# Performance work log

Hardware: AMD Instinct MI355X
Metric: run time of the kernel (lower is better)

## Reference

```python
import jax, jax.numpy as jnp
import numpy as np

N_NODES = 1000000
N_EDGES = 32000000
NUM_GRAPHS = 1024


def setup_inputs() -> dict:
    key = jax.random.key(0)
    k1, k2, k3, k4, k5 = jax.random.split(key, 5)
    x = jax.random.normal(k1, (N_NODES, 1), dtype=jnp.float32)
    W = jax.random.normal(k2, (1, 1), dtype=jnp.float32)
    b = jax.random.normal(k3, (1,), dtype=jnp.float32)
    edge_index = jax.random.randint(k4, (2, N_EDGES), 0, N_NODES, dtype=jnp.int64)
    batch = jnp.sort(jax.random.randint(k5, (N_NODES,), 0, NUM_GRAPHS, dtype=jnp.int64))
    return {"x": x, "W": W, "b": b, "edge_index": edge_index, "batch": batch}


def reference(x, W, b, edge_index, batch):
    src, dst = edge_index[0], edge_index[1]
    # SimpleConv (default sum aggregation): out[i] = sum_{(j->i) in E} x[j]
    agg = jax.ops.segment_sum(x[src], dst, num_segments=N_NODES)  # [N,1]
    h = jax.nn.relu(agg)
    # global_mean_pool over graph ids
    sums = jax.ops.segment_sum(h, batch, num_segments=NUM_GRAPHS)  # [G,1]
    counts = jax.ops.segment_sum(jnp.ones((N_NODES,), dtype=h.dtype), batch,
                                 num_segments=NUM_GRAPHS)  # [G]
    pooled = sums / jnp.maximum(counts, 1.0)[:, None]
    # Linear(1 -> 1): y = pooled @ W^T + b
    return pooled @ W.T + b
```

## Files before the change

kernel.cpp:

```cpp
#include <hip/hip_runtime.h>

#define N_NODES    1000000
#define N_EDGES    32000000
#define NUM_GRAPHS 1024

typedef int          vint4  __attribute__((ext_vector_type(4)));
typedef unsigned int uint32;
typedef unsigned int vuint4 __attribute__((ext_vector_type(4)));

#define BUCKET_SHIFT 12
#define BUCKET_NODES (1 << BUCKET_SHIFT)
#define NBUCKETS     245

#define T1_NCHUNK   512
#define T1_BLOCK    512
#define T1_EDGES_PER_CHUNK (N_EDGES / T1_NCHUNK)
#define T1_QUADS    (T1_EDGES_PER_CHUNK / 4)
#define T1_ROUNDS   ((T1_QUADS + T1_BLOCK - 1) / T1_BLOCK)
#define SCAP        64
#define SLAB_CAP    368

#define T2_CAP      136192
#define T2_NCHUNK   512
#define T2_EPC      (N_EDGES / T2_NCHUNK)

__global__ __launch_bounds__(T1_BLOCK)
void slab_scatter(const int* __restrict__ src,
                  const int* __restrict__ dst,
                  uint32* __restrict__ slab,
                  uint32* __restrict__ fcnt_g,
                  uint32* __restrict__ ecnt_g) {
    __shared__ uint32 stage[NBUCKETS][SCAP];
    __shared__ uint32 rpos[NBUCKETS];
    __shared__ uint32 ecnt[NBUCKETS];
    __shared__ uint32 flushed[NBUCKETS];
    __shared__ uint32 carry[NBUCKETS];

    const int tid = threadIdx.x;
    const int w   = blockIdx.x;
    const vint4* d4 = (const vint4*)(dst + (size_t)w * T1_EDGES_PER_CHUNK);
    const vint4* s4 = (const vint4*)(src + (size_t)w * T1_EDGES_PER_CHUNK);

    for (int b = tid; b < NBUCKETS; b += T1_BLOCK) {
        rpos[b] = 0; ecnt[b] = 0; flushed[b] = 0; carry[b] = 0;
    }
    __syncthreads();

    const int grp    = tid >> 4;
    const int lane16 = tid & 15;

    for (int r = 0; r < T1_ROUNDS; ++r) {
        int q = r * T1_BLOCK + tid;
        if (q < T1_QUADS) {
            vint4 d = d4[q];
            vint4 s = s4[q];
            #pragma unroll
            for (int k = 0; k < 4; ++k) {
                uint32 dd = (uint32)(k == 0 ? d.x : k == 1 ? d.y : k == 2 ? d.z : d.w);
                uint32 ss = (uint32)(k == 0 ? s.x : k == 1 ? s.y : k == 2 ? s.z : s.w);
                uint32 b  = dd >> BUCKET_SHIFT;
                uint32 v  = ((dd & (BUCKET_NODES - 1)) << 20) | ss;
                uint32 c  = carry[b] + atomicAdd(&rpos[b], 1u);
                if (c < SCAP) {
                    stage[b][c] = v;
                } else {
                    uint32 e = atomicAdd(&ecnt[b], 1u);
                    slab[((size_t)b * T1_NCHUNK + w) * SLAB_CAP + (SLAB_CAP - 1 - e)] = v;
                }
            }
        }
        __syncthreads();
        for (int b = grp; b < NBUCKETS; b += 32) {
            uint32 tot = carry[b] + rpos[b];
            if (tot > SCAP) tot = SCAP;
            uint32 lines = tot >> 4;
            uint32 rem   = tot & 15u;
            uint32 fl    = flushed[b];
            uint32* dp = slab + ((size_t)b * T1_NCHUNK + w) * SLAB_CAP + fl;
            for (uint32 l = 0; l < lines; ++l)
                dp[l * 16 + lane16] = stage[b][l * 16 + lane16];
            if (lines) {
                uint32 mv = 0;
                if (lane16 < rem) mv = stage[b][lines * 16 + lane16];
                if (lane16 < rem) stage[b][lane16] = mv;
            }
            if (lane16 == 0) {
                flushed[b] = fl + lines * 16;
                carry[b]   = rem;
                rpos[b]    = 0;
            }
        }
        __syncthreads();
    }
    for (int b = grp; b < NBUCKETS; b += 32) {
        uint32 rem = carry[b];
        uint32 fl  = flushed[b];
        uint32* dp = slab + ((size_t)b * T1_NCHUNK + w) * SLAB_CAP + fl;
        if (lane16 < rem) dp[lane16] = stage[b][lane16];
        if (lane16 == 0) {
            fcnt_g[(size_t)b * T1_NCHUNK + w] = fl + rem;
            ecnt_g[(size_t)b * T1_NCHUNK + w] = ecnt[b];
        }
    }
}

__global__ __launch_bounds__(1024)
void slab_reduce(const uint32* __restrict__ slab,
                 const uint32* __restrict__ fcnt_g,
                 const uint32* __restrict__ ecnt_g,
                 const float* __restrict__ x,
                 const int* __restrict__ batch,
                 float* __restrict__ sums,
                 float* __restrict__ counts) {
    __shared__ float acc[BUCKET_NODES];
    const int b = blockIdx.x;
    const int tid = threadIdx.x;
    for (int n = tid; n < BUCKET_NODES; n += 1024) acc[n] = 0.0f;
    __syncthreads();

    const int wv = tid >> 6, lane = tid & 63;
    for (int w = wv; w < T1_NCHUNK; w += 16) {
        size_t cell = (size_t)b * T1_NCHUNK + w;
        uint32 fc = fcnt_g[cell];
        uint32 ec = ecnt_g[cell];
        const uint32* base = slab + cell * SLAB_CAP;
        const vuint4* b4 = (const vuint4*)base;
        uint32 nq = fc >> 2;
        for (uint32 i = lane; i < nq; i += 64) {
            vuint4 v = b4[i];
            atomicAdd(&acc[v.x >> 20], x[v.x & 0xFFFFFu]);
            atomicAdd(&acc[v.y >> 20], x[v.y & 0xFFFFFu]);
            atomicAdd(&acc[v.z >> 20], x[v.z & 0xFFFFFu]);
            atomicAdd(&acc[v.w >> 20], x[v.w & 0xFFFFFu]);
        }
        for (uint32 i = nq * 4 + lane; i < fc; i += 64) {
            uint32 v = base[i];
            atomicAdd(&acc[v >> 20], x[v & 0xFFFFFu]);
        }
        for (uint32 i = lane; i < ec; i += 64) {
            uint32 v = base[SLAB_CAP - 1 - i];
            atomicAdd(&acc[v >> 20], x[v & 0xFFFFFu]);
        }
    }
    __syncthreads();

    const int node0 = b << BUCKET_SHIFT;
    for (int n = tid; n < BUCKET_NODES; n += 1024) {
        int i = node0 + n;
        float h = 0.0f;
        int g = -1;
        if (i < N_NODES) {
            h = fmaxf(acc[n], 0.0f);
            g = batch[i];
        }
        int g0 = __shfl(g, 0);
        if (__all(g == g0)) {
            #pragma unroll
            for (int off = 32; off > 0; off >>= 1)
                h += __shfl_down(h, off);
            if ((tid & 63) == 0 && g0 >= 0) {
                atomicAdd(&sums[g0], h);
                atomicAdd(&counts[g0], 64.0f);
            }
        } else if (g >= 0) {
            atomicAdd(&sums[g], h);
            atomicAdd(&counts[g], 1.0f);
        }
    }
}

__global__ void finalize_kernel(const float* __restrict__ sums,
                                const float* __restrict__ counts,
                                const float* __restrict__ W,
                                const float* __restrict__ b,
                                float* __restrict__ out) {
    int g = blockIdx.x * blockDim.x + threadIdx.x;
    if (g < NUM_GRAPHS) {
        float pooled = sums[g] / fmaxf(counts[g], 1.0f);
        out[g] = pooled * W[0] + b[0];
    }
}

__global__ __launch_bounds__(1024)
void bucket_scatter(const int* __restrict__ src,
                    const int* __restrict__ dst,
                    uint32* __restrict__ sorted,
                    uint32* __restrict__ gpos) {
    __shared__ uint32 hist[NBUCKETS];
    __shared__ uint32 pos[NBUCKETS];
    const int tid = threadIdx.x;
    const size_t base = (size_t)blockIdx.x * T2_EPC;
    for (int b = tid; b < NBUCKETS; b += 1024) hist[b] = 0;
    __syncthreads();
    const vint4* d4 = (const vint4*)(dst + base);
    const vint4* s4 = (const vint4*)(src + base);
    const int nvec = T2_EPC / 4;
    for (int i = tid; i < nvec; i += 1024) {
        vint4 d = d4[i];
        atomicAdd(&hist[(uint32)d.x >> BUCKET_SHIFT], 1u);
        atomicAdd(&hist[(uint32)d.y >> BUCKET_SHIFT], 1u);
        atomicAdd(&hist[(uint32)d.z >> BUCKET_SHIFT], 1u);
        atomicAdd(&hist[(uint32)d.w >> BUCKET_SHIFT], 1u);
    }
    __syncthreads();
    for (int b = tid; b < NBUCKETS; b += 1024)
        pos[b] = atomicAdd(&gpos[b], hist[b]);
    __syncthreads();
    for (int i = tid; i < nvec; i += 1024) {
        vint4 d = d4[i];
        vint4 s = s4[i];
        #pragma unroll
        for (int k = 0; k < 4; ++k) {
            uint32 dd = (uint32)(k == 0 ? d.x : k == 1 ? d.y : k == 2 ? d.z : d.w);
            uint32 ss = (uint32)(k == 0 ? s.x : k == 1 ? s.y : k == 2 ? s.z : s.w);
            uint32 b = dd >> BUCKET_SHIFT, dl = dd & (BUCKET_NODES - 1);
            uint32 slot = atomicAdd(&pos[b], 1u);
            if (slot < T2_CAP) sorted[(size_t)b * T2_CAP + slot] = (dl << 20) | ss;
        }
    }
}

__global__ __launch_bounds__(1024)
void bucket_reduce(const uint32* __restrict__ sorted,
                   const uint32* __restrict__ gpos,
                   const float* __restrict__ x,
                   const int* __restrict__ batch,
                   float* __restrict__ sums,
                   float* __restrict__ counts) {
    __shared__ float acc[BUCKET_NODES];
    const int b = blockIdx.x;
    const int tid = threadIdx.x;
    for (int n = tid; n < BUCKET_NODES; n += 1024) acc[n] = 0.0f;
    __syncthreads();
    uint32 cnt = gpos[b];
    if (cnt > T2_CAP) cnt = T2_CAP;
    const uint32* reg = sorted + (size_t)b * T2_CAP;
    const vuint4* r4 = (const vuint4*)reg;
    const uint32 nvec = cnt / 4;
    for (uint32 i = tid; i < nvec; i += 1024) {
        vuint4 v = r4[i];
        atomicAdd(&acc[v.x >> 20], x[v.x & 0xFFFFFu]);
        atomicAdd(&acc[v.y >> 20], x[v.y & 0xFFFFFu]);
        atomicAdd(&acc[v.z >> 20], x[v.z & 0xFFFFFu]);
        atomicAdd(&acc[v.w >> 20], x[v.w & 0xFFFFFu]);
    }
    for (uint32 i = nvec * 4 + tid; i < cnt; i += 1024) {
        uint32 v = reg[i];
        atomicAdd(&acc[v >> 20], x[v & 0xFFFFFu]);
    }
    __syncthreads();
    const int node0 = b << BUCKET_SHIFT;
    for (int n = tid; n < BUCKET_NODES; n += 1024) {
        int i = node0 + n;
        float h = 0.0f;
        int g = -1;
        if (i < N_NODES) {
            h = fmaxf(acc[n], 0.0f);
            g = batch[i];
        }
        int g0 = __shfl(g, 0);
        if (__all(g == g0)) {
            #pragma unroll
            for (int off = 32; off > 0; off >>= 1)
                h += __shfl_down(h, off);
            if ((tid & 63) == 0 && g0 >= 0) {
                atomicAdd(&sums[g0], h);
                atomicAdd(&counts[g0], 64.0f);
            }
        } else if (g >= 0) {
            atomicAdd(&sums[g], h);
            atomicAdd(&counts[g], 1.0f);
        }
    }
}

__global__ void scatter_edges_dev(const vint4* __restrict__ src4,
                                  const vint4* __restrict__ dst4,
                                  const float* __restrict__ x,
                                  float* __restrict__ agg) {
    int t = blockIdx.x * blockDim.x + threadIdx.x;
    if (t < N_EDGES / 4) {
        vint4 s = __builtin_nontemporal_load(&src4[t]);
        vint4 d = __builtin_nontemporal_load(&dst4[t]);
        atomicAdd(&agg[d.x], x[s.x]);
        atomicAdd(&agg[d.y], x[s.y]);
        atomicAdd(&agg[d.z], x[s.z]);
        atomicAdd(&agg[d.w], x[s.w]);
    }
}

__global__ void pool_nodes_kernel(const float* __restrict__ agg,
                                  const int* __restrict__ batch,
                                  float* __restrict__ sums,
                                  float* __restrict__ counts) {
    int i = blockIdx.x * blockDim.x + threadIdx.x;
    float h = 0.0f;
    int g = -1;
    if (i < N_NODES) {
        h = fmaxf(agg[i], 0.0f);
        g = batch[i];
    }
    int g0 = __shfl(g, 0);
    if (__all(g == g0)) {
        #pragma unroll
        for (int off = 32; off > 0; off >>= 1)
            h += __shfl_down(h, off);
        if ((threadIdx.x & 63) == 0 && g0 >= 0) {
            atomicAdd(&sums[g0], h);
            atomicAdd(&counts[g0], 64.0f);
        }
    } else if (g >= 0) {
        atomicAdd(&sums[g], h);
        atomicAdd(&counts[g], 1.0f);
    }
}

extern "C" void kernel_launch(void* const* d_in, const int* in_sizes, int n_in,
                              void* d_out, int out_size, void* d_ws, size_t ws_size,
                              hipStream_t stream) {
    const float* x     = (const float*)d_in[0];
    const float* W     = (const float*)d_in[1];
    const float* b     = (const float*)d_in[2];
    const int*   edge  = (const int*)d_in[3];
    const int*   batch = (const int*)d_in[4];
    float* out = (float*)d_out;

    const int* src = edge;
    const int* dst = edge + N_EDGES;

    const size_t ncells     = (size_t)NBUCKETS * T1_NCHUNK;
    const size_t slab_elems = ncells * SLAB_CAP;
    const size_t need1 = (slab_elems + 2 * ncells + 2 * NUM_GRAPHS) * 4;
    const size_t t2_elems = (size_t)NBUCKETS * T2_CAP;
    const size_t need2 = (t2_elems + 256 + 2 * NUM_GRAPHS) * 4;

    if (ws_size >= need1) {
        uint32* slab   = (uint32*)d_ws;
        uint32* fcnt_g = slab + slab_elems;
        uint32* ecnt_g = fcnt_g + ncells;
        float*  sums   = (float*)(ecnt_g + ncells);
        float*  counts = sums + NUM_GRAPHS;
        (void)hipMemsetAsync(sums, 0, 2 * NUM_GRAPHS * 4, stream);

        slab_scatter<<<T1_NCHUNK, T1_BLOCK, 0, stream>>>(src, dst, slab, fcnt_g, ecnt_g);
        slab_reduce<<<NBUCKETS, 1024, 0, stream>>>(slab, fcnt_g, ecnt_g, x, batch, sums, counts);
        finalize_kernel<<<(NUM_GRAPHS + 255) / 256, 256, 0, stream>>>(sums, counts, W, b, out);
    } else if (ws_size >= need2) {
        uint32* sorted = (uint32*)d_ws;
        uint32* gpos   = sorted + t2_elems;
        float*  sums   = (float*)(gpos + 256);
        float*  counts = sums + NUM_GRAPHS;
        (void)hipMemsetAsync(gpos, 0, (256 + 2 * NUM_GRAPHS) * 4, stream);

        bucket_scatter<<<T2_NCHUNK, 1024, 0, stream>>>(src, dst, sorted, gpos);
        bucket_reduce<<<NBUCKETS, 1024, 0, stream>>>(sorted, gpos, x, batch, sums, counts);
        finalize_kernel<<<(NUM_GRAPHS + 255) / 256, 256, 0, stream>>>(sums, counts, W, b, out);
    } else {
        float* agg    = (float*)d_ws;
        float* sums   = agg + N_NODES;
        float* counts = sums + NUM_GRAPHS;
        (void)hipMemsetAsync(d_ws, 0, ((size_t)N_NODES + 2 * NUM_GRAPHS) * 4, stream);

        int nthreads = N_EDGES / 4;
        scatter_edges_dev<<<(nthreads + 255) / 256, 256, 0, stream>>>(
            (const vint4*)src, (const vint4*)dst, x, agg);
        pool_nodes_kernel<<<(N_NODES + 255) / 256, 256, 0, stream>>>(agg, batch, sums, counts);
        finalize_kernel<<<(NUM_GRAPHS + 255) / 256, 256, 0, stream>>>(sums, counts, W, b, out);
    }
}
```

Before: 622.5 us.

## Split per-bucket slab reduction across four workgroups with global atomic merge

Adds a new reduce path that splits each node bucket's 512 slab cells across four workgroups, so there are 4x as many blocks (980 instead of 245) to fill the GPU. Each block accumulates partial sums in LDS and merges them into a global agg array with atomics. A separate pool_nodes_kernel then does the relu and mean-pool. This costs an extra memset, an extra kernel launch, global atomics and a second pass over the aggregated nodes. The path only runs if the workspace is large enough for the added agg buffer.

```diff
diff --git a/kernel.cpp b/kernel.cpp
--- a/kernel.cpp
+++ b/kernel.cpp
@@ -19,6 +19,9 @@
 #define T1_ROUNDS   ((T1_QUADS + T1_BLOCK - 1) / T1_BLOCK)
 #define SCAP        64
 #define SLAB_CAP    368
+
+#define RSPLIT        4
+#define CELLS_PER_WG  (T1_NCHUNK / RSPLIT)
 
 #define T2_CAP      136192
 #define T2_NCHUNK   512
@@ -105,6 +108,62 @@
 }
 
 __global__ __launch_bounds__(1024)
+void slab_reduce2(const uint32* __restrict__ slab,
+                  const uint32* __restrict__ fcnt_g,
+                  const uint32* __restrict__ ecnt_g,
+                  const float* __restrict__ x,
+                  float* __restrict__ agg) {
+    __shared__ float  acc[BUCKET_NODES];
+    __shared__ uint32 fc_s[CELLS_PER_WG];
+    __shared__ uint32 ec_s[CELLS_PER_WG];
+
+    const int b    = blockIdx.x / RSPLIT;
+    const int part = blockIdx.x % RSPLIT;
+    const int tid  = threadIdx.x;
+
+    for (int n = tid; n < BUCKET_NODES; n += 1024) acc[n] = 0.0f;
+    if (tid < CELLS_PER_WG) {
+        size_t cell = (size_t)b * T1_NCHUNK + (size_t)part * CELLS_PER_WG + tid;
+        fc_s[tid] = fcnt_g[cell];
+        ec_s[tid] = ecnt_g[cell];
+    }
+    __syncthreads();
+
+    const int wv = tid >> 6, lane = tid & 63;
+    for (int c = wv; c < CELLS_PER_WG; c += 16) {
+        const int w = part * CELLS_PER_WG + c;
+        const size_t cell = (size_t)b * T1_NCHUNK + w;
+        const uint32 fc = fc_s[c];
+        const uint32 ec = ec_s[c];
+        const uint32* base = slab + cell * SLAB_CAP;
+        const vuint4* b4 = (const vuint4*)base;
+        const uint32 nq = fc >> 2;
+        for (uint32 i = lane; i < nq; i += 64) {
+            vuint4 v = __builtin_nontemporal_load(&b4[i]);
+            atomicAdd(&acc[v.x >> 20], x[v.x & 0xFFFFFu]);
+            atomicAdd(&acc[v.y >> 20], x[v.y & 0xFFFFFu]);
+            atomicAdd(&acc[v.z >> 20], x[v.z & 0xFFFFFu]);
+            atomicAdd(&acc[v.w >> 20], x[v.w & 0xFFFFFu]);
+        }
+        for (uint32 i = nq * 4 + lane; i < fc; i += 64) {
+            uint32 v = __builtin_nontemporal_load(&base[i]);
+            atomicAdd(&acc[v >> 20], x[v & 0xFFFFFu]);
+        }
+        for (uint32 i = lane; i < ec; i += 64) {
+            uint32 v = base[SLAB_CAP - 1 - i];
+            atomicAdd(&acc[v >> 20], x[v & 0xFFFFFu]);
+        }
+    }
+    __syncthreads();
+
+    const int node0 = b << BUCKET_SHIFT;
+    for (int n = tid; n < BUCKET_NODES; n += 1024) {
+        float v = acc[n];
+        if (v != 0.0f) atomicAdd(&agg[node0 + n], v);
+    }
+}
+
+__global__ __launch_bounds__(1024)
 void slab_reduce(const uint32* __restrict__ slab,
                  const uint32* __restrict__ fcnt_g,
                  const uint32* __restrict__ ecnt_g,
@@ -330,11 +389,26 @@
 
     const size_t ncells     = (size_t)NBUCKETS * T1_NCHUNK;
     const size_t slab_elems = ncells * SLAB_CAP;
+    const size_t nagg       = (size_t)NBUCKETS * BUCKET_NODES;
+    const size_t need0 = (slab_elems + 2 * ncells + nagg + 2 * NUM_GRAPHS) * 4;
     const size_t need1 = (slab_elems + 2 * ncells + 2 * NUM_GRAPHS) * 4;
     const size_t t2_elems = (size_t)NBUCKETS * T2_CAP;
     const size_t need2 = (t2_elems + 256 + 2 * NUM_GRAPHS) * 4;
 
-    if (ws_size >= need1) {
+    if (ws_size >= need0) {
+        uint32* slab   = (uint32*)d_ws;
+        uint32* fcnt_g = slab + slab_elems;
+        uint32* ecnt_g = fcnt_g + ncells;
+        float*  agg    = (float*)(ecnt_g + ncells);
+        float*  sums   = agg + nagg;
+        float*  counts = sums + NUM_GRAPHS;
+        (void)hipMemsetAsync(agg, 0, (nagg + 2 * NUM_GRAPHS) * 4, stream);
+
+        slab_scatter<<<T1_NCHUNK, T1_BLOCK, 0, stream>>>(src, dst, slab, fcnt_g, ecnt_g);
+        slab_reduce2<<<NBUCKETS * RSPLIT, 1024, 0, stream>>>(slab, fcnt_g, ecnt_g, x, agg);
+        pool_nodes_kernel<<<(N_NODES + 255) / 256, 256, 0, stream>>>(agg, batch, sums, counts);
+        finalize_kernel<<<(NUM_GRAPHS + 255) / 256, 256, 0, stream>>>(sums, counts, W, b, out);
+    } else if (ws_size >= need1) {
         uint32* slab   = (uint32*)d_ws;
         uint32* fcnt_g = slab + slab_elems;
         uint32* ecnt_g = fcnt_g + ncells;
```

Result: slower. 650.1 us (+4.4%).

## Split slab reduction across four workgroups per bucket and add nontemporal memory ops

Applied to the files above, without the earlier changes.

The slab reduce now launches four workgroups per bucket, each handling a quarter of the chunk cells and interleaving four cells per wave. Each workgroup atomically adds its shared-memory partials into a global per-node aggregate, and a separate pooling kernel then applies relu and the per-graph mean. The goal is more parallelism and memory-level overlap in the reduce, which previously ran with only 245 workgroups. The scatter kernel now processes two quads per thread per round, uses nontemporal loads and stores, and adds overflow guards. The cost is an extra memset, global float atomics, an extra kernel launch and a larger workspace requirement.

```diff
diff --git a/kernel.cpp b/kernel.cpp
--- a/kernel.cpp
+++ b/kernel.cpp
@@ -16,9 +16,13 @@
 #define T1_BLOCK    512
 #define T1_EDGES_PER_CHUNK (N_EDGES / T1_NCHUNK)
 #define T1_QUADS    (T1_EDGES_PER_CHUNK / 4)
-#define T1_ROUNDS   ((T1_QUADS + T1_BLOCK - 1) / T1_BLOCK)
+#define T1_QPR      (2 * T1_BLOCK)
+#define T1_ROUNDS   ((T1_QUADS + T1_QPR - 1) / T1_QPR)
 #define SCAP        64
 #define SLAB_CAP    368
+
+#define RSPLIT        4
+#define CELLS_PER_WG  (T1_NCHUNK / RSPLIT)
 
 #define T2_CAP      136192
 #define T2_NCHUNK   512
@@ -50,25 +54,41 @@
     const int lane16 = tid & 15;
 
     for (int r = 0; r < T1_ROUNDS; ++r) {
-        int q = r * T1_BLOCK + tid;
-        if (q < T1_QUADS) {
-            vint4 d = d4[q];
-            vint4 s = s4[q];
-            #pragma unroll
-            for (int k = 0; k < 4; ++k) {
-                uint32 dd = (uint32)(k == 0 ? d.x : k == 1 ? d.y : k == 2 ? d.z : d.w);
-                uint32 ss = (uint32)(k == 0 ? s.x : k == 1 ? s.y : k == 2 ? s.z : s.w);
-                uint32 b  = dd >> BUCKET_SHIFT;
-                uint32 v  = ((dd & (BUCKET_NODES - 1)) << 20) | ss;
-                uint32 c  = carry[b] + atomicAdd(&rpos[b], 1u);
-                if (c < SCAP) {
-                    stage[b][c] = v;
-                } else {
-                    uint32 e = atomicAdd(&ecnt[b], 1u);
-                    slab[((size_t)b * T1_NCHUNK + w) * SLAB_CAP + (SLAB_CAP - 1 - e)] = v;
-                }
-            }
-        }
+        const int q0 = r * T1_QPR + tid;
+        const int q1 = q0 + T1_BLOCK;
+        const bool ok0 = q0 < T1_QUADS;
+        const bool ok1 = q1 < T1_QUADS;
+        vint4 d0, s0, d1, s1;
+        if (ok0) { d0 = __builtin_nontemporal_load(&d4[q0]);
+                   s0 = __builtin_nontemporal_load(&s4[q0]); }
+        if (ok1) { d1 = __builtin_nontemporal_load(&d4[q1]);
+                   s1 = __builtin_nontemporal_load(&s4[q1]); }
+
+#define SCAT4(dd4, ss4)                                                        \
+        {                                                                      \
+            _Pragma("unroll")                                                  \
+            for (int k = 0; k < 4; ++k) {                                      \
+                uint32 dd = (uint32)(k == 0 ? dd4.x : k == 1 ? dd4.y :         \
+                                     k == 2 ? dd4.z : dd4.w);                  \
+                uint32 ss = (uint32)(k == 0 ? ss4.x : k == 1 ? ss4.y :         \
+                                     k == 2 ? ss4.z : ss4.w);                  \
+                uint32 b  = dd >> BUCKET_SHIFT;                                \
+                uint32 v  = ((dd & (BUCKET_NODES - 1)) << 20) | ss;            \
+                uint32 c  = carry[b] + atomicAdd(&rpos[b], 1u);                \
+                if (c < SCAP) {                                                \
+                    stage[b][c] = v;                                           \
+                } else {                                                       \
+                    uint32 e = atomicAdd(&ecnt[b], 1u);                        \
+                    if (e < SLAB_CAP)          \
+                        __builtin_nontemporal_store(v,                         \
+                            &slab[((size_t)b * T1_NCHUNK + w) * SLAB_CAP       \
+                                  + (SLAB_CAP - 1 - e)]);                      \
+                }                                                              \
+            }                                                                  \
+        }
+        if (ok0) SCAT4(d0, s0)
+        if (ok1) SCAT4(d1, s1)
+#undef SCAT4
         __syncthreads();
         for (int b = grp; b < NBUCKETS; b += 32) {
             uint32 tot = carry[b] + rpos[b];
@@ -76,9 +96,12 @@
             uint32 lines = tot >> 4;
             uint32 rem   = tot & 15u;
             uint32 fl    = flushed[b];
+            uint32 maxl  = (SLAB_CAP > fl) ? ((SLAB_CAP - fl) >> 4) : 0u;
+            if (lines > maxl) lines = maxl;
             uint32* dp = slab + ((size_t)b * T1_NCHUNK + w) * SLAB_CAP + fl;
             for (uint32 l = 0; l < lines; ++l)
-                dp[l * 16 + lane16] = stage[b][l * 16 + lane16];
+                __builtin_nontemporal_store(stage[b][l * 16 + lane16],
+                                            &dp[l * 16 + lane16]);
             if (lines) {
                 uint32 mv = 0;
                 if (lane16 < rem) mv = stage[b][lines * 16 + lane16];
@@ -96,54 +119,188 @@
         uint32 rem = carry[b];
         uint32 fl  = flushed[b];
         uint32* dp = slab + ((size_t)b * T1_NCHUNK + w) * SLAB_CAP + fl;
-        if (lane16 < rem) dp[lane16] = stage[b][lane16];
+        if (lane16 < rem && fl + lane16 < SLAB_CAP)
+            __builtin_nontemporal_store(stage[b][lane16], &dp[lane16]);
         if (lane16 == 0) {
-            fcnt_g[(size_t)b * T1_NCHUNK + w] = fl + rem;
+            uint32 fc = fl + rem;
+            fcnt_g[(size_t)b * T1_NCHUNK + w] = fc > SLAB_CAP ? SLAB_CAP : fc;
             ecnt_g[(size_t)b * T1_NCHUNK + w] = ecnt[b];
         }
     }
 }
 
 __global__ __launch_bounds__(1024)
-void slab_reduce(const uint32* __restrict__ slab,
-                 const uint32* __restrict__ fcnt_g,
-                 const uint32* __restrict__ ecnt_g,
-                 const float* __restrict__ x,
-                 const int* __restrict__ batch,
-                 float* __restrict__ sums,
-                 float* __restrict__ counts) {
+void slab_reduce2(const uint32* __restrict__ slab,
+                  const uint32* __restrict__ fcnt_g,
+                  const uint32* __restrict__ ecnt_g,
+                  const float* __restrict__ x,
+                  float* __restrict__ agg) {
+    __shared__ float  acc[BUCKET_NODES];
+    __shared__ uint32 fc_s[CELLS_PER_WG];
+    __shared__ uint32 ec_s[CELLS_PER_WG];
+
+    const int b    = blockIdx.x / RSPLIT;
+    const int part = blockIdx.x % RSPLIT;
+    const int tid  = threadIdx.x;
+
+    for (int n = tid; n < BUCKET_NODES; n += 1024) acc[n] = 0.0f;
+    if (tid < CELLS_PER_WG) {
+        size_t cell = (size_t)b * T1_NCHUNK + (size_t)part * CELLS_PER_WG + tid;
+        uint32 fc = fcnt_g[cell];
+        uint32 ec = ecnt_g[cell];
+        if (fc > SLAB_CAP) fc = SLAB_CAP;
+        if (ec > SLAB_CAP) ec = SLAB_CAP;
+        fc_s[tid] = fc;
+        ec_s[tid] = ec;
+    }
+    __syncthreads();
+
+    const int wv = tid >> 6, lane = tid & 63;
+    for (int cp = wv; cp < CELLS_PER_WG; cp += 64) {
+        const int cA = cp, cB = cp + 16, cC = cp + 32, cD = cp + 48;
+        const uint32 fcA = fc_s[cA], fcB = fc_s[cB], fcC = fc_s[cC], fcD = fc_s[cD];
+        const uint32* baseA = slab + ((size_t)b * T1_NCHUNK + part * CELLS_PER_WG + cA) * SLAB_CAP;
+        const uint32* baseB = slab + ((size_t)b * T1_NCHUNK + part * CELLS_PER_WG + cB) * SLAB_CAP;
+        const uint32* baseC = slab + ((size_t)b * T1_NCHUNK + part * CELLS_PER_WG + cC) * SLAB_CAP;
+        const uint32* baseD = slab + ((size_t)b * T1_NCHUNK + part * CELLS_PER_WG + cD) * SLAB_CAP;
+        const uint32 nqA = fcA >> 2, nqB = fcB >> 2, nqC = fcC >> 2, nqD = fcD >> 2;
+        uint32 nqM = nqA;
+        if (nqB > nqM) nqM = nqB;
+        if (nqC > nqM) nqM = nqC;
+        if (nqD > nqM) nqM = nqD;
+
+        for (uint32 i = lane; i < nqM; i += 64) {
+            const bool aOK = i < nqA, bOK = i < nqB, cOK = i < nqC, dOK = i < nqD;
+            vuint4 va, vb, vc, vd;
+            if (aOK) va = __builtin_nontemporal_load(&((const vuint4*)baseA)[i]);
+            if (bOK) vb = __builtin_nontemporal_load(&((const vuint4*)baseB)[i]);
+            if (cOK) vc = __builtin_nontemporal_load(&((const vuint4*)baseC)[i]);
+            if (dOK) vd = __builtin_nontemporal_load(&((const vuint4*)baseD)[i]);
+            float xa0, xa1, xa2, xa3, xb0, xb1, xb2, xb3;
+            float xc0, xc1, xc2, xc3, xd0, xd1, xd2, xd3;
+            if (aOK) { xa0 = x[va.x & 0xFFFFFu]; xa1 = x[va.y & 0xFFFFFu];
+                       xa2 = x[va.z & 0xFFFFFu]; xa3 = x[va.w & 0xFFFFFu]; }
+            if (bOK) { xb0 = x[vb.x & 0xFFFFFu]; xb1 = x[vb.y & 0xFFFFFu];
+                       xb2 = x[vb.z & 0xFFFFFu]; xb3 = x[vb.w & 0xFFFFFu]; }
+            if (cOK) { xc0 = x[vc.x & 0xFFFFFu]; xc1 = x[vc.y & 0xFFFFFu];
+                       xc2 = x[vc.z & 0xFFFFFu]; xc3 = x[vc.w & 0xFFFFFu]; }
+            if (dOK) { xd0 = x[vd.x & 0xFFFFFu]; xd1 = x[vd.y & 0xFFFFFu];
+                       xd2 = x[vd.z & 0xFFFFFu]; xd3 = x[vd.w & 0xFFFFFu]; }
+            if (aOK) { atomicAdd(&acc[va.x >> 20], xa0); atomicAdd(&acc[va.y >> 20], xa1);
+                       atomicAdd(&acc[va.z >> 20], xa2); atomicAdd(&acc[va.w >> 20], xa3); }
+            if (bOK) { atomicAdd(&acc[vb.x >> 20], xb0); atomicAdd(&acc[vb.y >> 20], xb1);
+                       atomicAdd(&acc[vb.z >> 20], xb2); atomicAdd(&acc[vb.w >> 20], xb3); }
+            if (cOK) { atomicAdd(&acc[vc.x >> 20], xc0); atomicAdd(&acc[vc.y >> 20], xc1);
+                       atomicAdd(&acc[vc.z >> 20], xc2); atomicAdd(&acc[vc.w >> 20], xc3); }
+            if (dOK) { atomicAdd(&acc[vd.x >> 20], xd0); atomicAdd(&acc[vd.y >> 20], xd1);
+                       atomicAdd(&acc[vd.z >> 20], xd2); atomicAdd(&acc[vd.w >> 20], xd3); }
+        }
+#define REM(base, fc, ec)                                                      \
+        {                                                                      \
+            for (uint32 i = ((fc) & ~3u) + lane; i < (fc); i += 64) {          \
+                uint32 v = __builtin_nontemporal_load(&(base)[i]);             \
+                atomicAdd(&acc[v >> 20], x[v & 0xFFFFFu]);                     \
+            }                                                                  \
+            for (uint32 i = lane; i < (ec); i += 64) {                         \
+                uint32 v = (base)[SLAB_CAP - 1 - i];                           \
+                atomicAdd(&acc[v >> 20], x[v & 0xFFFFFu]);                     \
+            }                                                                  \
+        }
+        REM(baseA, fcA, ec_s[cA])
+        REM(baseB, fcB, ec_s[cB])
+        REM(baseC, fcC, ec_s[cC])
+        REM(baseD, fcD, ec_s[cD])
+#undef REM
+    }
+    __syncthreads();
+
+    const int node0 = b << BUCKET_SHIFT;
+    for (int n = tid; n < BUCKET_NODES; n += 1024) {
+        float v = acc[n];
+        if (v != 0.0f) atomicAdd(&agg[node0 + n], v);
+    }
+}
+
+__global__ void finalize_kernel(const float* __restrict__ sums,
+                                const float* __restrict__ counts,
+                                const float* __restrict__ W,
+                                const float* __restrict__ b,
+                                float* __restrict__ out) {
+    int g = blockIdx.x * blockDim.x + threadIdx.x;
+    if (g < NUM_GRAPHS) {
+        float pooled = sums[g] / fmaxf(counts[g], 1.0f);
+        out[g] = pooled * W[0] + b[0];
+    }
+}
+
+__global__ __launch_bounds__(1024)
+void bucket_scatter(const int* __restrict__ src,
+                    const int* __restrict__ dst,
+                    uint32* __restrict__ sorted,
+                    uint32* __restrict__ gpos) {
+    __shared__ uint32 hist[NBUCKETS];
+    __shared__ uint32 pos[NBUCKETS];
+    const int tid = threadIdx.x;
+    const size_t base = (size_t)blockIdx.x * T2_EPC;
+    for (int b = tid; b < NBUCKETS; b += 1024) hist[b] = 0;
+    __syncthreads();
+    const vint4* d4 = (const vint4*)(dst + base);
+    const vint4* s4 = (const vint4*)(src + base);
+    const int nvec = T2_EPC / 4;
+    for (int i = tid; i < nvec; i += 1024) {
+        vint4 d = d4[i];
+        atomicAdd(&hist[(uint32)d.x >> BUCKET_SHIFT], 1u);
+        atomicAdd(&hist[(uint32)d.y >> BUCKET_SHIFT], 1u);
+        atomicAdd(&hist[(uint32)d.z >> BUCKET_SHIFT], 1u);
+        atomicAdd(&hist[(uint32)d.w >> BUCKET_SHIFT], 1u);
+    }
+    __syncthreads();
+    for (int b = tid; b < NBUCKETS; b += 1024)
+        pos[b] = atomicAdd(&gpos[b], hist[b]);
+    __syncthreads();
+    for (int i = tid; i < nvec; i += 1024) {
+        vint4 d = d4[i];
+        vint4 s = s4[i];
+        #pragma unroll
+        for (int k = 0; k < 4; ++k) {
+            uint32 dd = (uint32)(k == 0 ? d.x : k == 1 ? d.y : k == 2 ? d.z : d.w);
+            uint32 ss = (uint32)(k == 0 ? s.x : k == 1 ? s.y : k == 2 ? s.z : s.w);
+            uint32 b = dd >> BUCKET_SHIFT, dl = dd & (BUCKET_NODES - 1);
+            uint32 slot = atomicAdd(&pos[b], 1u);
+            if (slot < T2_CAP) sorted[(size_t)b * T2_CAP + slot] = (dl << 20) | ss;
+        }
+    }
+}
+
+__global__ __launch_bounds__(1024)
+void bucket_reduce(const uint32* __restrict__ sorted,
+                   const uint32* __restrict__ gpos,
+                   const float* __restrict__ x,
+                   const int* __restrict__ batch,
+                   float* __restrict__ sums,
+                   float* __restrict__ counts) {
     __shared__ float acc[BUCKET_NODES];
     const int b = blockIdx.x;
     const int tid = threadIdx.x;
     for (int n = tid; n < BUCKET_NODES; n += 1024) acc[n] = 0.0f;
     __syncthreads();
-
-    const int wv = tid >> 6, lane = tid & 63;
-    for (int w = wv; w < T1_NCHUNK; w += 16) {
-        size_t cell = (size_t)b * T1_NCHUNK + w;
-        uint32 fc = fcnt_g[cell];
-        uint32 ec = ecnt_g[cell];
-        const uint32* base = slab + cell * SLAB_CAP;
-        const vuint4* b4 = (const vuint4*)base;
-        uint32 nq = fc >> 2;
-        for (uint32 i = lane; i < nq; i += 64) {
-            vuint4 v = b4[i];
-            atomicAdd(&acc[v.x >> 20], x[v.x & 0xFFFFFu]);
-            atomicAdd(&acc[v.y >> 20], x[v.y & 0xFFFFFu]);
-            atomicAdd(&acc[v.z >> 20], x[v.z & 0xFFFFFu]);
-            atomicAdd(&acc[v.w >> 20], x[v.w & 0xFFFFFu]);
-        }
-        for (uint32 i = nq * 4 + lane; i < fc; i += 64) {
-            uint32 v = base[i];
-            atomicAdd(&acc[v >> 20], x[v & 0xFFFFFu]);
-        }
-        for (uint32 i = lane; i < ec; i += 64) {
-            uint32 v = base[SLAB_CAP - 1 - i];
-            atomicAdd(&acc[v >> 20], x[v & 0xFFFFFu]);
-        }
-    }
-    __syncthreads();
-
+    uint32 cnt = gpos[b];
+    if (cnt > T2_CAP) cnt = T2_CAP;
+    const uint32* reg = sorted + (size_t)b * T2_CAP;
+    const vuint4* r4 = (const vuint4*)reg;
+    const uint32 nvec = cnt / 4;
+    for (uint32 i = tid; i < nvec; i += 1024) {
+        vuint4 v = r4[i];
+        atomicAdd(&acc[v.x >> 20], x[v.x & 0xFFFFFu]);
+        atomicAdd(&acc[v.y >> 20], x[v.y & 0xFFFFFu]);
+        atomicAdd(&acc[v.z >> 20], x[v.z & 0xFFFFFu]);
+        atomicAdd(&acc[v.w >> 20], x[v.w & 0xFFFFFu]);
+    }
+    for (uint32 i = nvec * 4 + tid; i < cnt; i += 1024) {
+        uint32 v = reg[i];
+        atomicAdd(&acc[v >> 20], x[v & 0xFFFFFu]);
+    }
+    __syncthreads();
     const int node0 = b << BUCKET_SHIFT;
     for (int n = tid; n < BUCKET_NODES; n += 1024) {
         int i = node0 + n;
@@ -169,111 +326,6 @@
     }
 }
 
-__global__ void finalize_kernel(const float* __restrict__ sums,
-                                const float* __restrict__ counts,
-                                const float* __restrict__ W,
-                                const float* __restrict__ b,
-                                float* __restrict__ out) {
-    int g = blockIdx.x * blockDim.x + threadIdx.x;
-    if (g < NUM_GRAPHS) {
-        float pooled = sums[g] / fmaxf(counts[g], 1.0f);
-        out[g] = pooled * W[0] + b[0];
-    }
-}
-
-__global__ __launch_bounds__(1024)
-void bucket_scatter(const int* __restrict__ src,
-                    const int* __restrict__ dst,
-                    uint32* __restrict__ sorted,
-                    uint32* __restrict__ gpos) {
-    __shared__ uint32 hist[NBUCKETS];
-    __shared__ uint32 pos[NBUCKETS];
-    const int tid = threadIdx.x;
-    const size_t base = (size_t)blockIdx.x * T2_EPC;
-    for (int b = tid; b < NBUCKETS; b += 1024) hist[b] = 0;
-    __syncthreads();
-    const vint4* d4 = (const vint4*)(dst + base);
-    const vint4* s4 = (const vint4*)(src + base);
-    const int nvec = T2_EPC / 4;
-    for (int i = tid; i < nvec; i += 1024) {
-        vint4 d = d4[i];
-        atomicAdd(&hist[(uint32)d.x >> BUCKET_SHIFT], 1u);
-        atomicAdd(&hist[(uint32)d.y >> BUCKET_SHIFT], 1u);
-        atomicAdd(&hist[(uint32)d.z >> BUCKET_SHIFT], 1u);
-        atomicAdd(&hist[(uint32)d.w >> BUCKET_SHIFT], 1u);
-    }
-    __syncthreads();
-    for (int b = tid; b < NBUCKETS; b += 1024)
-        pos[b] = atomicAdd(&gpos[b], hist[b]);
-    __syncthreads();
-    for (int i = tid; i < nvec; i += 1024) {
-        vint4 d = d4[i];
-        vint4 s = s4[i];
-        #pragma unroll
-        for (int k = 0; k < 4; ++k) {
-            uint32 dd = (uint32)(k == 0 ? d.x : k == 1 ? d.y : k == 2 ? d.z : d.w);
-            uint32 ss = (uint32)(k == 0 ? s.x : k == 1 ? s.y : k == 2 ? s.z : s.w);
-            uint32 b = dd >> BUCKET_SHIFT, dl = dd & (BUCKET_NODES - 1);
-            uint32 slot = atomicAdd(&pos[b], 1u);
-            if (slot < T2_CAP) sorted[(size_t)b * T2_CAP + slot] = (dl << 20) | ss;
-        }
-    }
-}
-
-__global__ __launch_bounds__(1024)
-void bucket_reduce(const uint32* __restrict__ sorted,
-                   const uint32* __restrict__ gpos,
-                   const float* __restrict__ x,
-                   const int* __restrict__ batch,
-                   float* __restrict__ sums,
-                   float* __restrict__ counts) {
-    __shared__ float acc[BUCKET_NODES];
-    const int b = blockIdx.x;
-    const int tid = threadIdx.x;
-    for (int n = tid; n < BUCKET_NODES; n += 1024) acc[n] = 0.0f;
-    __syncthreads();
-    uint32 cnt = gpos[b];
-    if (cnt > T2_CAP) cnt = T2_CAP;
-    const uint32* reg = sorted + (size_t)b * T2_CAP;
-    const vuint4* r4 = (const vuint4*)reg;
-    const uint32 nvec = cnt / 4;
-    for (uint32 i = tid; i < nvec; i += 1024) {
-        vuint4 v = r4[i];
-        atomicAdd(&acc[v.x >> 20], x[v.x & 0xFFFFFu]);
-        atomicAdd(&acc[v.y >> 20], x[v.y & 0xFFFFFu]);
-        atomicAdd(&acc[v.z >> 20], x[v.z & 0xFFFFFu]);
-        atomicAdd(&acc[v.w >> 20], x[v.w & 0xFFFFFu]);
-    }
-    for (uint32 i = nvec * 4 + tid; i < cnt; i += 1024) {
-        uint32 v = reg[i];
-        atomicAdd(&acc[v >> 20], x[v & 0xFFFFFu]);
-    }
-    __syncthreads();
-    const int node0 = b << BUCKET_SHIFT;
-    for (int n = tid; n < BUCKET_NODES; n += 1024) {
-        int i = node0 + n;
-        float h = 0.0f;
-        int g = -1;
-        if (i < N_NODES) {
-            h = fmaxf(acc[n], 0.0f);
-            g = batch[i];
-        }
-        int g0 = __shfl(g, 0);
-        if (__all(g == g0)) {
-            #pragma unroll
-            for (int off = 32; off > 0; off >>= 1)
-                h += __shfl_down(h, off);
-            if ((tid & 63) == 0 && g0 >= 0) {
-                atomicAdd(&sums[g0], h);
-                atomicAdd(&counts[g0], 64.0f);
-            }
-        } else if (g >= 0) {
-            atomicAdd(&sums[g], h);
-            atomicAdd(&counts[g], 1.0f);
-        }
-    }
-}
-
 __global__ void scatter_edges_dev(const vint4* __restrict__ src4,
                                   const vint4* __restrict__ dst4,
                                   const float* __restrict__ x,
@@ -330,20 +382,23 @@
 
     const size_t ncells     = (size_t)NBUCKETS * T1_NCHUNK;
     const size_t slab_elems = ncells * SLAB_CAP;
-    const size_t need1 = (slab_elems + 2 * ncells + 2 * NUM_GRAPHS) * 4;
+    const size_t nagg       = (size_t)NBUCKETS * BUCKET_NODES;
+    const size_t need0 = (slab_elems + 2 * ncells + nagg + 2 * NUM_GRAPHS) * 4;
     const size_t t2_elems = (size_t)NBUCKETS * T2_CAP;
     const size_t need2 = (t2_elems + 256 + 2 * NUM_GRAPHS) * 4;
 
-    if (ws_size >= need1) {
+    if (ws_size >= need0) {
         uint32* slab   = (uint32*)d_ws;
         uint32* fcnt_g = slab + slab_elems;
         uint32* ecnt_g = fcnt_g + ncells;
-        float*  sums   = (float*)(ecnt_g + ncells);
+        float*  agg    = (float*)(ecnt_g + ncells);
+        float*  sums   = agg + nagg;
         float*  counts = sums + NUM_GRAPHS;
-        (void)hipMemsetAsync(sums, 0, 2 * NUM_GRAPHS * 4, stream);
+        (void)hipMemsetAsync(agg, 0, (nagg + 2 * NUM_GRAPHS) * 4, stream);
 
         slab_scatter<<<T1_NCHUNK, T1_BLOCK, 0, stream>>>(src, dst, slab, fcnt_g, ecnt_g);
-        slab_reduce<<<NBUCKETS, 1024, 0, stream>>>(slab, fcnt_g, ecnt_g, x, batch, sums, counts);
+        slab_reduce2<<<NBUCKETS * RSPLIT, 1024, 0, stream>>>(slab, fcnt_g, ecnt_g, x, agg);
+        pool_nodes_kernel<<<(N_NODES + 255) / 256, 256, 0, stream>>>(agg, batch, sums, counts);
         finalize_kernel<<<(NUM_GRAPHS + 255) / 256, 256, 0, stream>>>(sums, counts, W, b, out);
     } else if (ws_size >= need2) {
         uint32* sorted = (uint32*)d_ws;
```

After: 659.9 us. 6.0% more time.
